# Optimization experiments

Measured on AMD Instinct MI355X. Metric: run time of the kernel, lower is better.

Reference implementation:

```python
import jax, jax.numpy as jnp
import numpy as np

NUM_ITERS = 3
NUM_SLOTS = 8
D = 128
MLP_HIDDEN = 128
EPS = 1e-8
LN_EPS = 1e-5
B, N = 64, 4096


def _layer_norm(x, g, b):
    m = jnp.mean(x, axis=-1, keepdims=True)
    v = jnp.mean(jnp.square(x - m), axis=-1, keepdims=True)
    return (x - m) * jax.lax.rsqrt(v + LN_EPS) * g + b


def setup_inputs() -> dict:
    key = jax.random.key(0)
    ks = jax.random.split(key, 16)
    s = 1.0 / np.sqrt(D)
    inp = {
        "x": jax.random.normal(ks[0], (B, N, D), jnp.float32),
        "slots_init": jax.random.normal(ks[1], (B, NUM_SLOTS, D), jnp.float32),
        "Wq": jax.random.normal(ks[2], (D, D), jnp.float32) * s,
        "bq": jnp.zeros((D,), jnp.float32),
        "Wk": jax.random.normal(ks[3], (D, D), jnp.float32) * s,
        "bk": jnp.zeros((D,), jnp.float32),
        "Wv": jax.random.normal(ks[4], (D, D), jnp.float32) * s,
        "bv": jnp.zeros((D,), jnp.float32),
        "g_in": jnp.ones((D,), jnp.float32), "b_in": jnp.zeros((D,), jnp.float32),
        "g_slot": jnp.ones((D,), jnp.float32), "b_slot": jnp.zeros((D,), jnp.float32),
        "g_mlp": jnp.ones((D,), jnp.float32), "b_mlp": jnp.zeros((D,), jnp.float32),
        "W1": jax.random.normal(ks[5], (MLP_HIDDEN, D), jnp.float32) * s,
        "b1": jnp.zeros((MLP_HIDDEN,), jnp.float32),
        "W2": jax.random.normal(ks[6], (D, MLP_HIDDEN), jnp.float32) * (1.0 / np.sqrt(MLP_HIDDEN)),
        "b2": jnp.zeros((D,), jnp.float32),
        "W_ih": jax.random.normal(ks[7], (3 * D, D), jnp.float32) * s,
        "W_hh": jax.random.normal(ks[8], (3 * D, D), jnp.float32) * s,
        "b_ih": jnp.zeros((3 * D,), jnp.float32),
        "b_hh": jnp.zeros((3 * D,), jnp.float32),
    }
    return inp


def _gru_cell(x, h, W_ih, W_hh, b_ih, b_hh):
    # torch.nn.GRUCell semantics
    gi = x @ W_ih.T + b_ih          # [.., 3D]
    gh = h @ W_hh.T + b_hh
    i_r, i_z, i_n = jnp.split(gi, 3, axis=-1)
    h_r, h_z, h_n = jnp.split(gh, 3, axis=-1)
    r = jax.nn.sigmoid(i_r + h_r)
    z = jax.nn.sigmoid(i_z + h_z)
    n = jnp.tanh(i_n + r * h_n)
    return (1.0 - z) * n + z * h


def reference(x, slots_init, Wq, bq, Wk, bk, Wv, bv, g_in, b_in, g_slot, b_slot,
              g_mlp, b_mlp, W1, b1, W2, b2, W_ih, W_hh, b_ih, b_hh):
    xn = _layer_norm(x, g_in, b_in)                 # [B,N,D]
    keys = xn @ Wk.T + bk                            # [B,N,D]
    values = xn @ Wv.T + bv                          # [B,N,D]
    scale = D ** -0.5
    slots = slots_init                               # [B,K,D]
    for _ in range(NUM_ITERS):
        prev = slots
        s = _layer_norm(slots, g_slot, b_slot)
        q = s @ Wq.T + bq                            # [B,K,D]
        logits = jnp.einsum('bid,bkd->bik', q, keys) * scale  # [B,K,N]
        attn = jax.nn.softmax(logits, axis=1)        # softmax over SLOT axis
        attn = attn + EPS
        attn = attn / jnp.sum(attn, axis=-1, keepdims=True)
        updates = jnp.einsum('bkd,bik->bid', values, attn)     # [B,K,D]
        slots = _gru_cell(updates.reshape(-1, D), prev.reshape(-1, D),
                          W_ih, W_hh, b_ih, b_hh).reshape(x.shape[0], -1, D)
        h = jax.nn.relu(_layer_norm(slots, g_mlp, b_mlp) @ W1.T + b1)
        slots = slots + (h @ W2.T + b2)
    return slots
```

## Files before the change

### kernel.cpp

```cpp
#include <hip/hip_runtime.h>
#include <hip/hip_bf16.h>

#define B_ 64
#define N_ 4096
#define KS 8
#define NCH 16
#define TP 136
#define LNEPS 1e-5f
#define EPSA 1e-8f
#define SCALE 0.08838834764831845f

typedef short short8  __attribute__((ext_vector_type(8)));
typedef short short4v __attribute__((ext_vector_type(4)));
typedef float f32x4   __attribute__((ext_vector_type(4)));

__device__ __forceinline__ unsigned short f2bf(float f) {
  union { float f; unsigned u; } v; v.f = f;
  unsigned r = v.u + 0x7fffu + ((v.u >> 16) & 1u);
  return (unsigned short)(r >> 16);
}
__device__ __forceinline__ float bflo(unsigned u) {
  union { unsigned u; float f; } c; c.u = u << 16; return c.f;
}
__device__ __forceinline__ float bfhi(unsigned u) {
  union { unsigned u; float f; } c; c.u = u & 0xffff0000u; return c.f;
}

__global__ __launch_bounds__(256) void prep_weights(
    const float* __restrict__ Wih, const float* __restrict__ Whh,
    const float* __restrict__ Wq,  const float* __restrict__ Wv,
    const float* __restrict__ W1,  const float* __restrict__ W2,
    float* __restrict__ WihT, float* __restrict__ WhhT,
    float* __restrict__ WqT,  float* __restrict__ WvT,
    float* __restrict__ W1T,  float* __restrict__ W2T)
{
  int id = blockIdx.x * 256 + threadIdx.x;
  if (id < 49152) {
    WihT[id] = Wih[(id % 384) * 128 + id / 384];
  } else if (id < 98304) {
    int k = id - 49152; WhhT[k] = Whh[(k % 384) * 128 + k / 384];
  } else if (id < 114688) {
    int k = id - 98304; WqT[k] = Wq[(k % 128) * 128 + k / 128];
  } else if (id < 131072) {
    int k = id - 114688; WvT[k] = Wv[(k % 128) * 128 + k / 128];
  } else if (id < 147456) {
    int k = id - 131072; W1T[k] = W1[(k % 128) * 128 + k / 128];
  } else if (id < 163840) {
    int k = id - 147456; W2T[k] = W2[(k % 128) * 128 + k / 128];
  }
}

__global__ __launch_bounds__(256) void q_init_kernel(
    const float* __restrict__ slots_in, const float* __restrict__ g_slot, const float* __restrict__ b_slot,
    const float* __restrict__ WqT, const float* __restrict__ bq,
    const float* __restrict__ Wk, const float* __restrict__ bk,
    float* __restrict__ qt, float* __restrict__ qc)
{
  __shared__ float sarr[128];
  __shared__ float qarr[128];
  int row = blockIdx.x, t = threadIdx.x;
  if (t < 64) {
    float a = slots_in[row*128 + t], b = slots_in[row*128 + 64 + t];
    float s = a + b, s2 = a*a + b*b;
    #pragma unroll
    for (int st = 1; st < 64; st <<= 1) { s += __shfl_xor(s, st); s2 += __shfl_xor(s2, st); }
    float mean = s * (1.f/128.f);
    float rstd = rsqrtf(s2 * (1.f/128.f) - mean*mean + LNEPS);
    sarr[t]    = (a - mean) * rstd * g_slot[t]    + b_slot[t];
    sarr[t+64] = (b - mean) * rstd * g_slot[t+64] + b_slot[t+64];
  }
  __syncthreads();
  if (t < 128) {
    float a = bq[t];
    for (int d = 0; d < 128; d++) a += sarr[d] * WqT[d*128 + t];
    qarr[t] = a;
  }
  __syncthreads();
  if (t < 128) {
    float a = 0.f;
    for (int j = 0; j < 128; j++) a += qarr[j] * Wk[j*128 + t];
    qt[row*128 + t] = a * SCALE;
  }
  if (t < 64) {
    float c = qarr[t]*bk[t] + qarr[t+64]*bk[t+64];
    #pragma unroll
    for (int st = 1; st < 64; st <<= 1) c += __shfl_xor(c, st);
    if (t == 0) qc[row] = c * SCALE;
  }
}

template<bool FUSE_LN>
__global__ __launch_bounds__(256) void attn_kernel(
    const float* __restrict__ x, const float* __restrict__ g_in, const float* __restrict__ b_in,
    unsigned short* __restrict__ xn,
    const float* __restrict__ qt, const float* __restrict__ qc,
    float* __restrict__ Upart, float* __restrict__ Spart)
{
  __shared__ __align__(16) unsigned short xt[4][16][TP];
  __shared__ __align__(16) float pb[4][16][8];
  __shared__ __align__(16) float ured[4][8][128];
  __shared__ __align__(16) float sred[4][8];

  const int tid = threadIdx.x;
  const int w = tid >> 6, lane = tid & 63;
  const int chunk = blockIdx.x, batch = blockIdx.y;
  const int m = lane & 15, quad = lane >> 4;

  short8 afrag[4];
  if (m < KS) {
    const float* qp = qt + (batch*KS + m)*128 + quad*8;
    #pragma unroll
    for (int kc = 0; kc < 4; kc++) {
      short8 a;
      #pragma unroll
      for (int j = 0; j < 8; j++) a[j] = (short)f2bf(qp[kc*32 + j]);
      afrag[kc] = a;
    }
  } else {
    #pragma unroll
    for (int kc = 0; kc < 4; kc++) {
      short8 a;
      #pragma unroll
      for (int j = 0; j < 8; j++) a[j] = 0;
      afrag[kc] = a;
    }
  }
  float creg[4];
  #pragma unroll
  for (int r = 0; r < 4; r++) creg[r] = qc[batch*KS + ((quad*4 + r) & 7)];

  float u0[8], u1[8], sac[4];
  #pragma unroll
  for (int i = 0; i < 8; i++) { u0[i] = 0.f; u1[i] = 0.f; }
  #pragma unroll
  for (int r = 0; r < 4; r++) sac[r] = 0.f;

  const int tok0 = chunk*256 + w*64;

  for (int g = 0; g < 4; g++) {
    const int tb = tok0 + g*16;
    if (FUSE_LN) {
      const int rw = lane >> 2, cp = lane & 3;
      const float* xrow = x + (size_t)(batch*N_ + tb + rw) * 128;
      float4 v[8];
      float s = 0.f, s2 = 0.f;
      #pragma unroll
      for (int i = 0; i < 8; i++) {
        v[i] = *(const float4*)(xrow + (cp + 4*i)*4);
        s  += v[i].x + v[i].y + v[i].z + v[i].w;
        s2 += v[i].x*v[i].x + v[i].y*v[i].y + v[i].z*v[i].z + v[i].w*v[i].w;
      }
      s += __shfl_xor(s, 1); s2 += __shfl_xor(s2, 1);
      s += __shfl_xor(s, 2); s2 += __shfl_xor(s2, 2);
      float mean = s * (1.f/128.f);
      float rstd = rsqrtf(s2 * (1.f/128.f) - mean*mean + LNEPS);
      #pragma unroll
      for (int i = 0; i < 8; i++) {
        int col = (cp + 4*i)*4;
        float4 gg = *(const float4*)(g_in + col);
        float4 bb = *(const float4*)(b_in + col);
        short4v pk;
        pk[0] = (short)f2bf((v[i].x - mean)*rstd*gg.x + bb.x);
        pk[1] = (short)f2bf((v[i].y - mean)*rstd*gg.y + bb.y);
        pk[2] = (short)f2bf((v[i].z - mean)*rstd*gg.z + bb.z);
        pk[3] = (short)f2bf((v[i].w - mean)*rstd*gg.w + bb.w);
        *(short4v*)&xt[w][rw][col] = pk;
      }
      #pragma unroll
      for (int p = 0; p < 4; p++) {
        int idx = p*64 + lane; int rr = idx >> 4, c16 = idx & 15;
        int4 dv = *(const int4*)&xt[w][rr][c16*8];
        *(int4*)(xn + (size_t)(batch*N_ + tb + rr)*128 + c16*8) = dv;
      }
    } else {
      #pragma unroll
      for (int p = 0; p < 4; p++) {
        int idx = p*64 + lane; int rr = idx >> 4, c16 = idx & 15;
        int4 dv = *(const int4*)(xn + (size_t)(batch*N_ + tb + rr)*128 + c16*8);
        *(int4*)&xt[w][rr][c16*8] = dv;
      }
    }

    f32x4 acc = {0.f, 0.f, 0.f, 0.f};
    #pragma unroll
    for (int kc = 0; kc < 4; kc++) {
      short8 bfrag = *(const short8*)&xt[w][m][kc*32 + quad*8];
      acc = __builtin_amdgcn_mfma_f32_16x16x32_bf16(afrag[kc], bfrag, acc, 0, 0, 0);
    }
    float l[4], o[4];
    #pragma unroll
    for (int r = 0; r < 4; r++) l[r] = acc[r] + creg[r];
    #pragma unroll
    for (int r = 0; r < 4; r++) o[r] = __shfl_xor(l[r], 16);
    float mx = fmaxf(fmaxf(fmaxf(l[0], l[1]), fmaxf(l[2], l[3])),
                     fmaxf(fmaxf(o[0], o[1]), fmaxf(o[2], o[3])));
    float e0 = __expf(l[0]-mx), e1 = __expf(l[1]-mx), e2 = __expf(l[2]-mx), e3 = __expf(l[3]-mx);
    float den = e0+e1+e2+e3 + __expf(o[0]-mx)+__expf(o[1]-mx)+__expf(o[2]-mx)+__expf(o[3]-mx);
    float rd = 1.f / den;
    float p0 = e0*rd + EPSA, p1 = e1*rd + EPSA, p2 = e2*rd + EPSA, p3 = e3*rd + EPSA;
    sac[0] += p0; sac[1] += p1; sac[2] += p2; sac[3] += p3;
    if (lane < 32) {
      float4 pv; pv.x = p0; pv.y = p1; pv.z = p2; pv.w = p3;
      *(float4*)&pb[w][m][quad*4] = pv;
    }

    #pragma unroll
    for (int t = 0; t < 16; t++) {
      float4 pA = *(const float4*)&pb[w][t][0];
      float4 pB = *(const float4*)&pb[w][t][4];
      unsigned vp = *(const unsigned*)&xt[w][t][lane*2];
      float f0 = bflo(vp), f1 = bfhi(vp);
      u0[0] += pA.x*f0; u1[0] += pA.x*f1;
      u0[1] += pA.y*f0; u1[1] += pA.y*f1;
      u0[2] += pA.z*f0; u1[2] += pA.z*f1;
      u0[3] += pA.w*f0; u1[3] += pA.w*f1;
      u0[4] += pB.x*f0; u1[4] += pB.x*f1;
      u0[5] += pB.y*f0; u1[5] += pB.y*f1;
      u0[6] += pB.z*f0; u1[6] += pB.z*f1;
      u0[7] += pB.w*f0; u1[7] += pB.w*f1;
    }
  }

  #pragma unroll
  for (int st = 1; st < 16; st <<= 1) {
    #pragma unroll
    for (int r = 0; r < 4; r++) sac[r] += __shfl_xor(sac[r], st);
  }
  if (lane == 0)  { sred[w][0]=sac[0]; sred[w][1]=sac[1]; sred[w][2]=sac[2]; sred[w][3]=sac[3]; }
  if (lane == 16) { sred[w][4]=sac[0]; sred[w][5]=sac[1]; sred[w][6]=sac[2]; sred[w][7]=sac[3]; }
  #pragma unroll
  for (int i = 0; i < 8; i++)
    *(float2*)&ured[w][i][lane*2] = make_float2(u0[i], u1[i]);
  __syncthreads();

  {
    const float* ur = &ured[0][0][0];
    int i4 = tid * 4;
    float4 a = *(const float4*)(ur + i4);
    float4 b = *(const float4*)(ur + 1024 + i4);
    float4 c = *(const float4*)(ur + 2048 + i4);
    float4 d = *(const float4*)(ur + 3072 + i4);
    float4 o4;
    o4.x = a.x+b.x+c.x+d.x; o4.y = a.y+b.y+c.y+d.y;
    o4.z = a.z+b.z+c.z+d.z; o4.w = a.w+b.w+c.w+d.w;
    *(float4*)(Upart + (size_t)(batch*NCH + chunk)*1024 + i4) = o4;
    if (tid < 8)
      Spart[(batch*NCH + chunk)*8 + tid] =
        sred[0][tid] + sred[1][tid] + sred[2][tid] + sred[3][tid];
  }
}

__global__ __launch_bounds__(256) void update_kernel(
    const float* __restrict__ slots_in, float* __restrict__ slots_out,
    const float* __restrict__ Upart, const float* __restrict__ Spart,
    const float* __restrict__ WvT, const float* __restrict__ bv,
    const float* __restrict__ WihT, const float* __restrict__ WhhT,
    const float* __restrict__ b_ih, const float* __restrict__ b_hh,
    const float* __restrict__ g_mlp, const float* __restrict__ b_mlp,
    const float* __restrict__ W1T, const float* __restrict__ b1,
    const float* __restrict__ W2T, const float* __restrict__ b2,
    const float* __restrict__ g_slot, const float* __restrict__ b_slot,
    const float* __restrict__ WqT, const float* __restrict__ bq,
    const float* __restrict__ Wk, const float* __restrict__ bk,
    float* __restrict__ qt, float* __restrict__ qc)
{
  __shared__ float bu[128], su[128], hb[128];
  __shared__ float gi[384], gh[384];
  __shared__ float s1[128], smv[128], hmv[128], s2v[128], sqv[128], qa[128];
  __shared__ float stats[2];
  int row = blockIdx.x, t = threadIdx.x;
  int batch = row >> 3, slot = row & 7;

  if (t < 128) {
    float ua = 0.f;
    #pragma unroll 4
    for (int c = 0; c < 16; c++) ua += Upart[(size_t)((batch*16 + c)*8 + slot)*128 + t];
    float ss = 0.f;
    #pragma unroll 4
    for (int c = 0; c < 16; c++) ss += Spart[(batch*16 + c)*8 + slot];
    bu[t] = ua / ss;
    hb[t] = slots_in[row*128 + t];
  }
  __syncthreads();
  if (t < 128) {
    float a = bv[t];
    for (int d = 0; d < 128; d++) a += bu[d] * WvT[d*128 + t];
    su[t] = a;
  }
  __syncthreads();
  #pragma unroll
  for (int p = 0; p < 3; p++) {
    int tau = t + p*256;
    if (tau < 768) {
      bool ismat = tau >= 384;
      int j = ismat ? (tau - 384) : tau;
      const float* WT  = ismat ? WhhT : WihT;
      const float* vec = ismat ? hb : su;
      float a = ismat ? b_hh[j] : b_ih[j];
      for (int d = 0; d < 128; d++) a += vec[d] * WT[d*384 + j];
      if (ismat) gh[j] = a; else gi[j] = a;
    }
  }
  __syncthreads();
  if (t < 128) {
    float r = 1.f / (1.f + __expf(-(gi[t] + gh[t])));
    float z = 1.f / (1.f + __expf(-(gi[128+t] + gh[128+t])));
    float n = tanhf(gi[256+t] + r * gh[256+t]);
    s1[t] = (1.f - z)*n + z*hb[t];
  }
  __syncthreads();
  if (t < 64) {
    float a = s1[t], b = s1[t+64];
    float s = a + b, s2 = a*a + b*b;
    #pragma unroll
    for (int st = 1; st < 64; st <<= 1) { s += __shfl_xor(s, st); s2 += __shfl_xor(s2, st); }
    if (t == 0) { float mean = s*(1.f/128.f); stats[0] = mean;
                  stats[1] = rsqrtf(s2*(1.f/128.f) - mean*mean + LNEPS); }
  }
  __syncthreads();
  if (t < 128) smv[t] = (s1[t] - stats[0])*stats[1]*g_mlp[t] + b_mlp[t];
  __syncthreads();
  if (t < 128) {
    float a = b1[t];
    for (int d = 0; d < 128; d++) a += smv[d]*W1T[d*128 + t];
    hmv[t] = fmaxf(a, 0.f);
  }
  __syncthreads();
  if (t < 128) {
    float a = s1[t] + b2[t];
    for (int d = 0; d < 128; d++) a += hmv[d]*W2T[d*128 + t];
    s2v[t] = a;
    slots_out[row*128 + t] = a;
  }
  __syncthreads();
  if (t < 64) {
    float a = s2v[t], b = s2v[t+64];
    float s = a + b, s2 = a*a + b*b;
    #pragma unroll
    for (int st = 1; st < 64; st <<= 1) { s += __shfl_xor(s, st); s2 += __shfl_xor(s2, st); }
    if (t == 0) { float mean = s*(1.f/128.f); stats[0] = mean;
                  stats[1] = rsqrtf(s2*(1.f/128.f) - mean*mean + LNEPS); }
  }
  __syncthreads();
  if (t < 128) sqv[t] = (s2v[t] - stats[0])*stats[1]*g_slot[t] + b_slot[t];
  __syncthreads();
  if (t < 128) {
    float a = bq[t];
    for (int d = 0; d < 128; d++) a += sqv[d]*WqT[d*128 + t];
    qa[t] = a;
  }
  __syncthreads();
  if (t < 128) {
    float a = 0.f;
    for (int j = 0; j < 128; j++) a += qa[j]*Wk[j*128 + t];
    qt[row*128 + t] = a * SCALE;
  }
  if (t < 64) {
    float c = qa[t]*bk[t] + qa[t+64]*bk[t+64];
    #pragma unroll
    for (int st = 1; st < 64; st <<= 1) c += __shfl_xor(c, st);
    if (t == 0) qc[row] = c * SCALE;
  }
}

extern "C" void kernel_launch(void* const* d_in, const int* in_sizes, int n_in,
                              void* d_out, int out_size, void* d_ws, size_t ws_size,
                              hipStream_t stream) {
  const float* x          = (const float*)d_in[0];
  const float* slots_init = (const float*)d_in[1];
  const float* Wq   = (const float*)d_in[2];
  const float* bq   = (const float*)d_in[3];
  const float* Wk   = (const float*)d_in[4];
  const float* bk   = (const float*)d_in[5];
  const float* Wv   = (const float*)d_in[6];
  const float* bv   = (const float*)d_in[7];
  const float* g_in = (const float*)d_in[8];
  const float* b_in = (const float*)d_in[9];
  const float* g_slot = (const float*)d_in[10];
  const float* b_slot = (const float*)d_in[11];
  const float* g_mlp  = (const float*)d_in[12];
  const float* b_mlp  = (const float*)d_in[13];
  const float* W1   = (const float*)d_in[14];
  const float* b1   = (const float*)d_in[15];
  const float* W2   = (const float*)d_in[16];
  const float* b2   = (const float*)d_in[17];
  const float* Wih  = (const float*)d_in[18];
  const float* Whh  = (const float*)d_in[19];
  const float* b_ih = (const float*)d_in[20];
  const float* b_hh = (const float*)d_in[21];

  char* p = (char*)d_ws;
  unsigned short* xn = (unsigned short*)p; p += (size_t)B_*N_*128*2;
  float* qt    = (float*)p; p += (size_t)B_*KS*128*4;
  float* qc    = (float*)p; p += (size_t)B_*KS*4 + 2048;
  float* slots = (float*)p; p += (size_t)B_*KS*128*4;
  float* Upart = (float*)p; p += (size_t)B_*NCH*KS*128*4;
  float* Spart = (float*)p; p += (size_t)B_*NCH*KS*4 + 2048;
  float* WihT  = (float*)p; p += 49152*4;
  float* WhhT  = (float*)p; p += 49152*4;
  float* WqT   = (float*)p; p += 16384*4;
  float* WvT   = (float*)p; p += 16384*4;
  float* W1T   = (float*)p; p += 16384*4;
  float* W2T   = (float*)p; p += 16384*4;

  prep_weights<<<640, 256, 0, stream>>>(Wih, Whh, Wq, Wv, W1, W2,
                                        WihT, WhhT, WqT, WvT, W1T, W2T);
  q_init_kernel<<<512, 256, 0, stream>>>(slots_init, g_slot, b_slot, WqT, bq, Wk, bk, qt, qc);

  attn_kernel<true><<<dim3(NCH, B_), 256, 0, stream>>>(x, g_in, b_in, xn, qt, qc, Upart, Spart);
  update_kernel<<<512, 256, 0, stream>>>(slots_init, slots, Upart, Spart,
      WvT, bv, WihT, WhhT, b_ih, b_hh, g_mlp, b_mlp, W1T, b1, W2T, b2,
      g_slot, b_slot, WqT, bq, Wk, bk, qt, qc);

  attn_kernel<false><<<dim3(NCH, B_), 256, 0, stream>>>(x, g_in, b_in, xn, qt, qc, Upart, Spart);
  update_kernel<<<512, 256, 0, stream>>>(slots, slots, Upart, Spart,
      WvT, bv, WihT, WhhT, b_ih, b_hh, g_mlp, b_mlp, W1T, b1, W2T, b2,
      g_slot, b_slot, WqT, bq, Wk, bk, qt, qc);

  attn_kernel<false><<<dim3(NCH, B_), 256, 0, stream>>>(x, g_in, b_in, xn, qt, qc, Upart, Spart);
  update_kernel<<<512, 256, 0, stream>>>(slots, (float*)d_out, Upart, Spart,
      WvT, bv, WihT, WhhT, b_ih, b_hh, g_mlp, b_mlp, W1T, b1, W2T, b2,
      g_slot, b_slot, WqT, bq, Wk, bk, qt, qc);

  (void)in_sizes; (void)n_in; (void)out_size; (void)ws_size;
}
```

Baseline: 403.3 us.

## Split attention over more token chunks and merge GRU gate weights

```diff
diff --git a/kernel.cpp b/kernel.cpp
--- a/kernel.cpp
+++ b/kernel.cpp
@@ -4,7 +4,7 @@
 #define B_ 64
 #define N_ 4096
 #define KS 8
-#define NCH 16
+#define NCH 64
 #define TP 136
 #define LNEPS 1e-5f
 #define EPSA 1e-8f
@@ -25,20 +25,19 @@
 __device__ __forceinline__ float bfhi(unsigned u) {
   union { unsigned u; float f; } c; c.u = u & 0xffff0000u; return c.f;
 }
+__device__ __forceinline__ float sigmf(float x) { return 1.f / (1.f + __expf(-x)); }
 
 __global__ __launch_bounds__(256) void prep_weights(
     const float* __restrict__ Wih, const float* __restrict__ Whh,
     const float* __restrict__ Wq,  const float* __restrict__ Wv,
     const float* __restrict__ W1,  const float* __restrict__ W2,
-    float* __restrict__ WihT, float* __restrict__ WhhT,
-    float* __restrict__ WqT,  float* __restrict__ WvT,
-    float* __restrict__ W1T,  float* __restrict__ W2T)
+    float* __restrict__ WgT, float* __restrict__ WqT,
+    float* __restrict__ WvT, float* __restrict__ W1T, float* __restrict__ W2T)
 {
   int id = blockIdx.x * 256 + threadIdx.x;
-  if (id < 49152) {
-    WihT[id] = Wih[(id % 384) * 128 + id / 384];
-  } else if (id < 98304) {
-    int k = id - 49152; WhhT[k] = Whh[(k % 384) * 128 + k / 384];
+  if (id < 98304) {
+    int d = id / 768, j = id % 768;
+    WgT[id] = (j < 384) ? Wih[j*128 + d] : Whh[(j-384)*128 + d];
   } else if (id < 114688) {
     int k = id - 98304; WqT[k] = Wq[(k % 128) * 128 + k / 128];
   } else if (id < 131072) {
@@ -96,15 +95,18 @@
     const float* __restrict__ qt, const float* __restrict__ qc,
     float* __restrict__ Upart, float* __restrict__ Spart)
 {
-  __shared__ __align__(16) unsigned short xt[4][16][TP];
+  __shared__ union ShMem {
+    unsigned short xt[4][16][TP];
+    float ured[4][8][128];
+  } sh;
   __shared__ __align__(16) float pb[4][16][8];
-  __shared__ __align__(16) float ured[4][8][128];
-  __shared__ __align__(16) float sred[4][8];
+  __shared__ float sred[4][8];
 
   const int tid = threadIdx.x;
   const int w = tid >> 6, lane = tid & 63;
   const int chunk = blockIdx.x, batch = blockIdx.y;
   const int m = lane & 15, quad = lane >> 4;
+  const int tb = (chunk*4 + w)*16;
 
   short8 afrag[4];
   if (m < KS) {
@@ -129,96 +131,90 @@
   #pragma unroll
   for (int r = 0; r < 4; r++) creg[r] = qc[batch*KS + ((quad*4 + r) & 7)];
 
-  float u0[8], u1[8], sac[4];
+  short8 bfrag[4];
+  if (FUSE_LN) {
+    const int rw = lane >> 2, cp = lane & 3;
+    const float* xrow = x + (size_t)(batch*N_ + tb + rw) * 128;
+    float4 v[8];
+    float s = 0.f, s2 = 0.f;
+    #pragma unroll
+    for (int i = 0; i < 8; i++) {
+      v[i] = *(const float4*)(xrow + (cp + 4*i)*4);
+      s  += v[i].x + v[i].y + v[i].z + v[i].w;
+      s2 += v[i].x*v[i].x + v[i].y*v[i].y + v[i].z*v[i].z + v[i].w*v[i].w;
+    }
+    s += __shfl_xor(s, 1); s2 += __shfl_xor(s2, 1);
+    s += __shfl_xor(s, 2); s2 += __shfl_xor(s2, 2);
+    float mean = s * (1.f/128.f);
+    float rstd = rsqrtf(s2 * (1.f/128.f) - mean*mean + LNEPS);
+    #pragma unroll
+    for (int i = 0; i < 8; i++) {
+      int col = (cp + 4*i)*4;
+      float4 gg = *(const float4*)(g_in + col);
+      float4 bb = *(const float4*)(b_in + col);
+      short4v pk;
+      pk[0] = (short)f2bf((v[i].x - mean)*rstd*gg.x + bb.x);
+      pk[1] = (short)f2bf((v[i].y - mean)*rstd*gg.y + bb.y);
+      pk[2] = (short)f2bf((v[i].z - mean)*rstd*gg.z + bb.z);
+      pk[3] = (short)f2bf((v[i].w - mean)*rstd*gg.w + bb.w);
+      *(short4v*)&sh.xt[w][rw][col] = pk;
+    }
+    #pragma unroll
+    for (int p = 0; p < 4; p++) {
+      int idx = p*64 + lane; int rr = idx >> 4, c16 = idx & 15;
+      int4 dv = *(const int4*)&sh.xt[w][rr][c16*8];
+      *(int4*)(xn + (size_t)(batch*N_ + tb + rr)*128 + c16*8) = dv;
+    }
+    #pragma unroll
+    for (int kc = 0; kc < 4; kc++)
+      bfrag[kc] = *(const short8*)&sh.xt[w][m][kc*32 + quad*8];
+  } else {
+    const unsigned short* xp = xn + (size_t)(batch*N_ + tb + m)*128;
+    #pragma unroll
+    for (int kc = 0; kc < 4; kc++) {
+      bfrag[kc] = *(const short8*)(xp + kc*32 + quad*8);
+      *(short8*)&sh.xt[w][m][kc*32 + quad*8] = bfrag[kc];
+    }
+  }
+
+  f32x4 acc = {0.f, 0.f, 0.f, 0.f};
+  #pragma unroll
+  for (int kc = 0; kc < 4; kc++)
+    acc = __builtin_amdgcn_mfma_f32_16x16x32_bf16(afrag[kc], bfrag[kc], acc, 0, 0, 0);
+  float l[4], o[4];
+  #pragma unroll
+  for (int r = 0; r < 4; r++) l[r] = acc[r] + creg[r];
+  #pragma unroll
+  for (int r = 0; r < 4; r++) o[r] = __shfl_xor(l[r], 16);
+  float mx = fmaxf(fmaxf(fmaxf(l[0], l[1]), fmaxf(l[2], l[3])),
+                   fmaxf(fmaxf(o[0], o[1]), fmaxf(o[2], o[3])));
+  float e0 = __expf(l[0]-mx), e1 = __expf(l[1]-mx), e2 = __expf(l[2]-mx), e3 = __expf(l[3]-mx);
+  float den = e0+e1+e2+e3 + __expf(o[0]-mx)+__expf(o[1]-mx)+__expf(o[2]-mx)+__expf(o[3]-mx);
+  float rd = 1.f / den;
+  float p0 = e0*rd + EPSA, p1 = e1*rd + EPSA, p2 = e2*rd + EPSA, p3 = e3*rd + EPSA;
+  float sac[4] = {p0, p1, p2, p3};
+  if (lane < 32) {
+    float4 pv; pv.x = p0; pv.y = p1; pv.z = p2; pv.w = p3;
+    *(float4*)&pb[w][m][quad*4] = pv;
+  }
+
+  float u0[8], u1[8];
   #pragma unroll
   for (int i = 0; i < 8; i++) { u0[i] = 0.f; u1[i] = 0.f; }
   #pragma unroll
-  for (int r = 0; r < 4; r++) sac[r] = 0.f;
-
-  const int tok0 = chunk*256 + w*64;
-
-  for (int g = 0; g < 4; g++) {
-    const int tb = tok0 + g*16;
-    if (FUSE_LN) {
-      const int rw = lane >> 2, cp = lane & 3;
-      const float* xrow = x + (size_t)(batch*N_ + tb + rw) * 128;
-      float4 v[8];
-      float s = 0.f, s2 = 0.f;
-      #pragma unroll
-      for (int i = 0; i < 8; i++) {
-        v[i] = *(const float4*)(xrow + (cp + 4*i)*4);
-        s  += v[i].x + v[i].y + v[i].z + v[i].w;
-        s2 += v[i].x*v[i].x + v[i].y*v[i].y + v[i].z*v[i].z + v[i].w*v[i].w;
-      }
-      s += __shfl_xor(s, 1); s2 += __shfl_xor(s2, 1);
-      s += __shfl_xor(s, 2); s2 += __shfl_xor(s2, 2);
-      float mean = s * (1.f/128.f);
-      float rstd = rsqrtf(s2 * (1.f/128.f) - mean*mean + LNEPS);
-      #pragma unroll
-      for (int i = 0; i < 8; i++) {
-        int col = (cp + 4*i)*4;
-        float4 gg = *(const float4*)(g_in + col);
-        float4 bb = *(const float4*)(b_in + col);
-        short4v pk;
-        pk[0] = (short)f2bf((v[i].x - mean)*rstd*gg.x + bb.x);
-        pk[1] = (short)f2bf((v[i].y - mean)*rstd*gg.y + bb.y);
-        pk[2] = (short)f2bf((v[i].z - mean)*rstd*gg.z + bb.z);
-        pk[3] = (short)f2bf((v[i].w - mean)*rstd*gg.w + bb.w);
-        *(short4v*)&xt[w][rw][col] = pk;
-      }
-      #pragma unroll
-      for (int p = 0; p < 4; p++) {
-        int idx = p*64 + lane; int rr = idx >> 4, c16 = idx & 15;
-        int4 dv = *(const int4*)&xt[w][rr][c16*8];
-        *(int4*)(xn + (size_t)(batch*N_ + tb + rr)*128 + c16*8) = dv;
-      }
-    } else {
-      #pragma unroll
-      for (int p = 0; p < 4; p++) {
-        int idx = p*64 + lane; int rr = idx >> 4, c16 = idx & 15;
-        int4 dv = *(const int4*)(xn + (size_t)(batch*N_ + tb + rr)*128 + c16*8);
-        *(int4*)&xt[w][rr][c16*8] = dv;
-      }
-    }
-
-    f32x4 acc = {0.f, 0.f, 0.f, 0.f};
-    #pragma unroll
-    for (int kc = 0; kc < 4; kc++) {
-      short8 bfrag = *(const short8*)&xt[w][m][kc*32 + quad*8];
-      acc = __builtin_amdgcn_mfma_f32_16x16x32_bf16(afrag[kc], bfrag, acc, 0, 0, 0);
-    }
-    float l[4], o[4];
-    #pragma unroll
-    for (int r = 0; r < 4; r++) l[r] = acc[r] + creg[r];
-    #pragma unroll
-    for (int r = 0; r < 4; r++) o[r] = __shfl_xor(l[r], 16);
-    float mx = fmaxf(fmaxf(fmaxf(l[0], l[1]), fmaxf(l[2], l[3])),
-                     fmaxf(fmaxf(o[0], o[1]), fmaxf(o[2], o[3])));
-    float e0 = __expf(l[0]-mx), e1 = __expf(l[1]-mx), e2 = __expf(l[2]-mx), e3 = __expf(l[3]-mx);
-    float den = e0+e1+e2+e3 + __expf(o[0]-mx)+__expf(o[1]-mx)+__expf(o[2]-mx)+__expf(o[3]-mx);
-    float rd = 1.f / den;
-    float p0 = e0*rd + EPSA, p1 = e1*rd + EPSA, p2 = e2*rd + EPSA, p3 = e3*rd + EPSA;
-    sac[0] += p0; sac[1] += p1; sac[2] += p2; sac[3] += p3;
-    if (lane < 32) {
-      float4 pv; pv.x = p0; pv.y = p1; pv.z = p2; pv.w = p3;
-      *(float4*)&pb[w][m][quad*4] = pv;
-    }
-
-    #pragma unroll
-    for (int t = 0; t < 16; t++) {
-      float4 pA = *(const float4*)&pb[w][t][0];
-      float4 pB = *(const float4*)&pb[w][t][4];
-      unsigned vp = *(const unsigned*)&xt[w][t][lane*2];
-      float f0 = bflo(vp), f1 = bfhi(vp);
-      u0[0] += pA.x*f0; u1[0] += pA.x*f1;
-      u0[1] += pA.y*f0; u1[1] += pA.y*f1;
-      u0[2] += pA.z*f0; u1[2] += pA.z*f1;
-      u0[3] += pA.w*f0; u1[3] += pA.w*f1;
-      u0[4] += pB.x*f0; u1[4] += pB.x*f1;
-      u0[5] += pB.y*f0; u1[5] += pB.y*f1;
-      u0[6] += pB.z*f0; u1[6] += pB.z*f1;
-      u0[7] += pB.w*f0; u1[7] += pB.w*f1;
-    }
+  for (int t = 0; t < 16; t++) {
+    float4 pA = *(const float4*)&pb[w][t][0];
+    float4 pB = *(const float4*)&pb[w][t][4];
+    unsigned vp = *(const unsigned*)&sh.xt[w][t][lane*2];
+    float f0 = bflo(vp), f1 = bfhi(vp);
+    u0[0] += pA.x*f0; u1[0] += pA.x*f1;
+    u0[1] += pA.y*f0; u1[1] += pA.y*f1;
+    u0[2] += pA.z*f0; u1[2] += pA.z*f1;
+    u0[3] += pA.w*f0; u1[3] += pA.w*f1;
+    u0[4] += pB.x*f0; u1[4] += pB.x*f1;
+    u0[5] += pB.y*f0; u1[5] += pB.y*f1;
+    u0[6] += pB.z*f0; u1[6] += pB.z*f1;
+    u0[7] += pB.w*f0; u1[7] += pB.w*f1;
   }
 
   #pragma unroll
@@ -228,13 +224,15 @@
   }
   if (lane == 0)  { sred[w][0]=sac[0]; sred[w][1]=sac[1]; sred[w][2]=sac[2]; sred[w][3]=sac[3]; }
   if (lane == 16) { sred[w][4]=sac[0]; sred[w][5]=sac[1]; sred[w][6]=sac[2]; sred[w][7]=sac[3]; }
+
+  __syncthreads();
   #pragma unroll
   for (int i = 0; i < 8; i++)
-    *(float2*)&ured[w][i][lane*2] = make_float2(u0[i], u1[i]);
+    *(float2*)&sh.ured[w][i][lane*2] = make_float2(u0[i], u1[i]);
   __syncthreads();
 
   {
-    const float* ur = &ured[0][0][0];
+    const float* ur = &sh.ured[0][0][0];
     int i4 = tid * 4;
     float4 a = *(const float4*)(ur + i4);
     float4 b = *(const float4*)(ur + 1024 + i4);
@@ -254,7 +252,7 @@
     const float* __restrict__ slots_in, float* __restrict__ slots_out,
     const float* __restrict__ Upart, const float* __restrict__ Spart,
     const float* __restrict__ WvT, const float* __restrict__ bv,
-    const float* __restrict__ WihT, const float* __restrict__ WhhT,
+    const float* __restrict__ WgT,
     const float* __restrict__ b_ih, const float* __restrict__ b_hh,
     const float* __restrict__ g_mlp, const float* __restrict__ b_mlp,
     const float* __restrict__ W1T, const float* __restrict__ b1,
@@ -265,22 +263,30 @@
     float* __restrict__ qt, float* __restrict__ qc)
 {
   __shared__ float bu[128], su[128], hb[128];
-  __shared__ float gi[384], gh[384];
+  __shared__ float gg[768];
   __shared__ float s1[128], smv[128], hmv[128], s2v[128], sqv[128], qa[128];
-  __shared__ float stats[2];
+  __shared__ float up2[2][128];
+  __shared__ float stats[2], sSum;
   int row = blockIdx.x, t = threadIdx.x;
   int batch = row >> 3, slot = row & 7;
 
-  if (t < 128) {
+  {
+    int d = t & 127, h = t >> 7;
+    const float* Up = Upart + ((size_t)(batch*NCH + h*32)*8 + slot)*128 + d;
     float ua = 0.f;
-    #pragma unroll 4
-    for (int c = 0; c < 16; c++) ua += Upart[(size_t)((batch*16 + c)*8 + slot)*128 + t];
-    float ss = 0.f;
-    #pragma unroll 4
-    for (int c = 0; c < 16; c++) ss += Spart[(batch*16 + c)*8 + slot];
-    bu[t] = ua / ss;
-    hb[t] = slots_in[row*128 + t];
-  }
+    #pragma unroll 8
+    for (int c = 0; c < 32; c++) ua += Up[(size_t)c*1024];
+    up2[h][d] = ua;
+  }
+  if (t < 64) {
+    float sv = Spart[(batch*NCH + t)*8 + slot];
+    #pragma unroll
+    for (int st = 1; st < 64; st <<= 1) sv += __shfl_xor(sv, st);
+    if (t == 0) sSum = sv;
+  }
+  if (t >= 64 && t < 192) hb[t-64] = slots_in[row*128 + (t-64)];
+  __syncthreads();
+  if (t < 128) bu[t] = (up2[0][t] + up2[1][t]) / sSum;
   __syncthreads();
   if (t < 128) {
     float a = bv[t];
@@ -288,24 +294,25 @@
     su[t] = a;
   }
   __syncthreads();
-  #pragma unroll
-  for (int p = 0; p < 3; p++) {
-    int tau = t + p*256;
-    if (tau < 768) {
-      bool ismat = tau >= 384;
-      int j = ismat ? (tau - 384) : tau;
-      const float* WT  = ismat ? WhhT : WihT;
-      const float* vec = ismat ? hb : su;
-      float a = ismat ? b_hh[j] : b_ih[j];
-      for (int d = 0; d < 128; d++) a += vec[d] * WT[d*384 + j];
-      if (ismat) gh[j] = a; else gi[j] = a;
-    }
-  }
-  __syncthreads();
-  if (t < 128) {
-    float r = 1.f / (1.f + __expf(-(gi[t] + gh[t])));
-    float z = 1.f / (1.f + __expf(-(gi[128+t] + gh[128+t])));
-    float n = tanhf(gi[256+t] + r * gh[256+t]);
+  {
+    float a0 = b_ih[t];
+    float a1 = (t < 128) ? b_ih[256+t] : b_hh[t-128];
+    float a2 = b_hh[t+128];
+    const float* v1p = (t < 128) ? su : hb;
+    for (int d = 0; d < 128; d++) {
+      float sd = su[d], hd = hb[d], vd = v1p[d];
+      const float* wr = WgT + d*768 + t;
+      a0 += sd * wr[0];
+      a1 += vd * wr[256];
+      a2 += hd * wr[512];
+    }
+    gg[t] = a0; gg[t+256] = a1; gg[t+512] = a2;
+  }
+  __syncthreads();
+  if (t < 128) {
+    float r = sigmf(gg[t] + gg[384+t]);
+    float z = sigmf(gg[128+t] + gg[512+t]);
+    float n = tanhf(gg[256+t] + r * gg[640+t]);
     s1[t] = (1.f - z)*n + z*hb[t];
   }
   __syncthreads();
@@ -396,30 +403,29 @@
   float* slots = (float*)p; p += (size_t)B_*KS*128*4;
   float* Upart = (float*)p; p += (size_t)B_*NCH*KS*128*4;
   float* Spart = (float*)p; p += (size_t)B_*NCH*KS*4 + 2048;
-  float* WihT  = (float*)p; p += 49152*4;
-  float* WhhT  = (float*)p; p += 49152*4;
+  float* WgT   = (float*)p; p += 98304*4;
   float* WqT   = (float*)p; p += 16384*4;
   float* WvT   = (float*)p; p += 16384*4;
   float* W1T   = (float*)p; p += 16384*4;
   float* W2T   = (float*)p; p += 16384*4;
 
   prep_weights<<<640, 256, 0, stream>>>(Wih, Whh, Wq, Wv, W1, W2,
-                                        WihT, WhhT, WqT, WvT, W1T, W2T);
+                                        WgT, WqT, WvT, W1T, W2T);
   q_init_kernel<<<512, 256, 0, stream>>>(slots_init, g_slot, b_slot, WqT, bq, Wk, bk, qt, qc);
 
   attn_kernel<true><<<dim3(NCH, B_), 256, 0, stream>>>(x, g_in, b_in, xn, qt, qc, Upart, Spart);
   update_kernel<<<512, 256, 0, stream>>>(slots_init, slots, Upart, Spart,
-      WvT, bv, WihT, WhhT, b_ih, b_hh, g_mlp, b_mlp, W1T, b1, W2T, b2,
+      WvT, bv, WgT, b_ih, b_hh, g_mlp, b_mlp, W1T, b1, W2T, b2,
       g_slot, b_slot, WqT, bq, Wk, bk, qt, qc);
 
   attn_kernel<false><<<dim3(NCH, B_), 256, 0, stream>>>(x, g_in, b_in, xn, qt, qc, Upart, Spart);
   update_kernel<<<512, 256, 0, stream>>>(slots, slots, Upart, Spart,
-      WvT, bv, WihT, WhhT, b_ih, b_hh, g_mlp, b_mlp, W1T, b1, W2T, b2,
+      WvT, bv, WgT, b_ih, b_hh, g_mlp, b_mlp, W1T, b1, W2T, b2,
       g_slot, b_slot, WqT, bq, Wk, bk, qt, qc);
 
   attn_kernel<false><<<dim3(NCH, B_), 256, 0, stream>>>(x, g_in, b_in, xn, qt, qc, Upart, Spart);
   update_kernel<<<512, 256, 0, stream>>>(slots, (float*)d_out, Upart, Spart,
-      WvT, bv, WihT, WhhT, b_ih, b_hh, g_mlp, b_mlp, W1T, b1, W2T, b2,
+      WvT, bv, WgT, b_ih, b_hh, g_mlp, b_mlp, W1T, b1, W2T, b2,
       g_slot, b_slot, WqT, bq, Wk, bk, qt, qc);
 
   (void)in_sizes; (void)n_in; (void)out_size; (void)ws_size;
```

Result: faster. 394.7 us (-2.1%).
